# Kernel optimization log

Hardware: AMD Instinct MI355X
Metric: run time of the kernel (lower is better)

## Reference

```python
import jax, jax.numpy as jnp
import numpy as np

B, S = 2, 2048          # packed prefill: 2 sequences of 2048 tokens
T = B * S
HID = 3584
H, KV, D = 16, 8, 256   # query heads, kv heads, head_dim (num_groups = 2)
SCALE = 256.0 ** -0.5   # query_pre_attn_scalar ** -0.5
SOFTCAP = 50.0
WINDOW = 1024           # sliding_window (window_size_left)
ROPE_THETA = 10000.0


def _rope_cos_sin():
    # TGI PositionRotaryEmbedding: per-token cos/sin of shape [T, D//2]
    inv_freq = 1.0 / (ROPE_THETA ** (np.arange(0, D, 2, dtype=np.float32) / D))
    pos = np.tile(np.arange(S, dtype=np.float32), B)  # positions restart per sequence
    freqs = pos[:, None] * inv_freq[None, :]          # [T, D/2]
    return jnp.asarray(np.cos(freqs)), jnp.asarray(np.sin(freqs))


def _apply_rope(x, cos, sin):
    # neox-style rotate-half; x: [T, h, D], cos/sin: [T, D/2]
    x1, x2 = x[..., : D // 2], x[..., D // 2 :]
    c, s = cos[:, None, :], sin[:, None, :]
    return jnp.concatenate([x1 * c - x2 * s, x2 * c + x1 * s], axis=-1)


def setup_inputs() -> dict:
    key = jax.random.key(0)
    k1, k2, k3 = jax.random.split(key, 3)
    cos, sin = _rope_cos_sin()
    return {
        "hidden_states": jax.random.normal(k1, (T, HID), dtype=jnp.float32),
        "cos": cos,
        "sin": sin,
        "w_qkv": jax.random.normal(k2, ((H + 2 * KV) * D, HID), dtype=jnp.float32) * 0.02,
        "w_o": jax.random.normal(k3, (HID, H * D), dtype=jnp.float32) * 0.02,
    }


def reference(hidden_states, cos, sin, w_qkv, w_o):
    qkv = hidden_states @ w_qkv.T                      # [T, (H+2KV)*D]
    q = qkv[:, : H * D].reshape(T, H, D)
    k = qkv[:, H * D : (H + KV) * D].reshape(T, KV, D)
    v = qkv[:, (H + KV) * D :].reshape(T, KV, D)

    q = _apply_rope(q, cos, sin)
    k = _apply_rope(k, cos, sin)

    # unpack varlen batch (equal-length sequences)
    q = q.reshape(B, S, H, D)
    # GQA: repeat each kv head num_groups=2 times (kv_head_mapping)
    k = jnp.repeat(k.reshape(B, S, KV, D), H // KV, axis=2)
    v = jnp.repeat(v.reshape(B, S, KV, D), H // KV, axis=2)

    scores = jnp.einsum("bqhd,bkhd->bhqk", q, k) * SCALE
    scores = SOFTCAP * jnp.tanh(scores / SOFTCAP)      # logit softcapping

    i = jnp.arange(S)[:, None]
    j = jnp.arange(S)[None, :]
    allowed = (j <= i) & (j >= i - WINDOW)             # causal + sliding window left
    scores = jnp.where(allowed[None, None], scores, jnp.finfo(scores.dtype).min)

    probs = jax.nn.softmax(scores, axis=-1)
    out = jnp.einsum("bhqk,bkhd->bqhd", probs, v)      # [B, S, H, D]
    return out.reshape(T, H * D) @ w_o.T               # [T, HID]
```

## Files before the change

### kernel.cpp

```cpp
#include <hip/hip_runtime.h>

typedef __bf16 bf16x8 __attribute__((ext_vector_type(8)));
typedef __bf16 bf16x4 __attribute__((ext_vector_type(4)));
typedef float  f32x4  __attribute__((ext_vector_type(4)));

#define AS1 __attribute__((address_space(1)))
#define AS3 __attribute__((address_space(3)))

__device__ __forceinline__ void async16(const void* g, void* l) {
  __builtin_amdgcn_global_load_lds((const AS1 void*)g, (AS3 void*)l, 16, 0, 0);
}

static constexpr int T_   = 4096;
static constexpr int Sq   = 2048;
static constexpr int HID  = 3584;
static constexpr int NH   = 16;
static constexpr int NKV  = 8;
static constexpr int DH   = 256;
static constexpr float SCALE_   = 0.0625f;
static constexpr float SOFTCAP_ = 50.0f;
static constexpr int WINDOW_    = 1024;

__global__ __launch_bounds__(256) void cast2_f32_bf16(const float4* __restrict__ a,
                                                      bf16x4* __restrict__ oa, int n4a,
                                                      const float4* __restrict__ b,
                                                      bf16x4* __restrict__ ob, int n4b) {
  int i = blockIdx.x * 256 + threadIdx.x;
  int stride = gridDim.x * 256;
  int ntot = n4a + n4b;
  for (; i < ntot; i += stride) {
    const float4 v = (i < n4a) ? a[i] : b[i - n4a];
    bf16x4 o;
    o[0] = (__bf16)v.x; o[1] = (__bf16)v.y; o[2] = (__bf16)v.z; o[3] = (__bf16)v.w;
    if (i < n4a) oa[i] = o; else ob[i - n4a] = o;
  }
}

template <bool OUT_BF16>
__global__ __launch_bounds__(256) void gemm_bt(const __bf16* __restrict__ A,
                                               const __bf16* __restrict__ B,
                                               __bf16* __restrict__ Cb,
                                               float* __restrict__ Cf,
                                               int M, int N, int K) {
  __shared__ __bf16 lA[128 * 64];
  __shared__ __bf16 lB[128 * 64];
  const int tid  = threadIdx.x;
  const int w    = tid >> 6;
  const int lane = tid & 63;
  const int mrow = lane & 15;
  const int quad = lane >> 4;
  const int sw   = mrow & 7;
  const int tileN = blockIdx.x * 128;
  const int tileM = blockIdx.y * 128;
  const int wr = (w >> 1) * 64;
  const int wc = (w & 1) * 64;

  f32x4 acc[4][4];
#pragma unroll
  for (int i = 0; i < 4; ++i)
#pragma unroll
    for (int j = 0; j < 4; ++j) acc[i][j] = (f32x4){0.f, 0.f, 0.f, 0.f};

  const int rsub = tid >> 3;
  const int usw  = (tid & 7) ^ (rsub & 7);
  const int ccol = usw * 8;

  for (int k0 = 0; k0 < K; k0 += 64) {
#pragma unroll
    for (int it = 0; it < 4; ++it) {
      int row = it * 32 + rsub;
      const __bf16* ga = A + (size_t)(tileM + row) * K + k0 + ccol;
      const __bf16* gb = B + (size_t)(tileN + row) * K + k0 + ccol;
      async16(ga, &lA[(it * 256 + w * 64) * 8]);
      async16(gb, &lB[(it * 256 + w * 64) * 8]);
    }
    __syncthreads();
#pragma unroll
    for (int kk = 0; kk < 2; ++kk) {
      bf16x8 af[4], bfr[4];
#pragma unroll
      for (int i = 0; i < 4; ++i)
        af[i] = *(const bf16x8*)&lA[(wr + i * 16 + mrow) * 64 + (((kk * 4 + quad) ^ sw) * 8)];
#pragma unroll
      for (int j = 0; j < 4; ++j)
        bfr[j] = *(const bf16x8*)&lB[(wc + j * 16 + mrow) * 64 + (((kk * 4 + quad) ^ sw) * 8)];
#pragma unroll
      for (int i = 0; i < 4; ++i)
#pragma unroll
        for (int j = 0; j < 4; ++j)
          acc[i][j] = __builtin_amdgcn_mfma_f32_16x16x32_bf16(af[i], bfr[j], acc[i][j], 0, 0, 0);
    }
    __syncthreads();
  }

#pragma unroll
  for (int i = 0; i < 4; ++i) {
    int row0 = tileM + wr + i * 16 + quad * 4;
#pragma unroll
    for (int j = 0; j < 4; ++j) {
      int col = tileN + wc + j * 16 + mrow;
#pragma unroll
      for (int r = 0; r < 4; ++r) {
        if constexpr (OUT_BF16)
          Cb[(size_t)(row0 + r) * N + col] = (__bf16)acc[i][j][r];
        else
          Cf[(size_t)(row0 + r) * N + col] = acc[i][j][r];
      }
    }
  }
}

__global__ __launch_bounds__(256) void aux_fused(const __bf16* __restrict__ qkv,
                                                 const float* __restrict__ cosb,
                                                 const float* __restrict__ sinb,
                                                 __bf16* __restrict__ qout,
                                                 __bf16* __restrict__ kout,
                                                 __bf16* __restrict__ vt,
                                                 const float4* __restrict__ wo,
                                                 bf16x4* __restrict__ wo_bf) {
  __shared__ __bf16 tile[64][72];
  const int blk = blockIdx.x;
  const int tid = threadIdx.x;

  if (blk < 4096) {
    const int t = blk;
    const int b = t >> 11, s = t & (Sq - 1);
    const int d = tid & 127;
    const int half = tid >> 7;
    const float c  = cosb[t * 128 + d];
    const float sn = sinb[t * 128 + d];
    const size_t base = (size_t)t * 8192;
#pragma unroll
    for (int it = 0; it < 12; ++it) {
      int seg = it * 2 + half;
      float x1 = (float)qkv[base + seg * 256 + d];
      float x2 = (float)qkv[base + seg * 256 + 128 + d];
      float o1 = x1 * c - x2 * sn;
      float o2 = x2 * c + x1 * sn;
      if (seg < 16) {
        size_t o = ((size_t)(b * NH + seg) * Sq + s) * DH + d;
        qout[o] = (__bf16)o1;
        qout[o + 128] = (__bf16)o2;
      } else {
        int kvh = seg - 16;
        size_t o = ((size_t)(b * NKV + kvh) * Sq + s) * DH + d;
        kout[o] = (__bf16)o1;
        kout[o + 128] = (__bf16)o2;
      }
    }
  } else if (blk < 6144) {
    const int flat = blk - 4096;
    const int bx  = flat & 127;
    const int bkv = flat >> 7;
    const int b = bkv >> 3, kv = bkv & 7;
    const int st0 = (bx >> 2) * 64;
    const int dt0 = (bx & 3) * 64;
#pragma unroll
    for (int it = 0; it < 2; ++it) {
      int g = it * 256 + tid;
      int r = g >> 3, cc = (g & 7) * 8;
      const __bf16* src = qkv + (size_t)(b * Sq + st0 + r) * 8192 + 6144 + kv * 256 + dt0 + cc;
      bf16x8 v = *(const bf16x8*)src;
#pragma unroll
      for (int j = 0; j < 8; ++j) tile[r][cc + j] = v[j];
    }
    __syncthreads();
#pragma unroll
    for (int it = 0; it < 2; ++it) {
      int g = it * 256 + tid;
      int r = g >> 3, cc = (g & 7) * 8;
      bf16x8 v;
#pragma unroll
      for (int j = 0; j < 8; ++j) v[j] = tile[cc + j][r];
      *(bf16x8*)(vt + ((size_t)bkv * DH + dt0 + r) * Sq + st0 + cc) = v;
    }
  } else {
    const int n4 = HID * 4096 / 4;
    int i = (blk - 6144) * 256 + tid;
    const int stride = 1024 * 256;
    for (; i < n4; i += stride) {
      float4 v = wo[i];
      bf16x4 o;
      o[0] = (__bf16)v.x; o[1] = (__bf16)v.y; o[2] = (__bf16)v.z; o[3] = (__bf16)v.w;
      wo_bf[i] = o;
    }
  }
}

template <int MODE>
__device__ __forceinline__ void softcap_tile(const f32x4 sc[4], float lrun[4],
                                             __bf16* Pl, int pbase, int mrow,
                                             int kt, int qi) {
#pragma unroll
  for (int j = 0; j < 4; ++j) {
    const int kj = kt + j * 16 + mrow;
#pragma unroll
    for (int r = 0; r < 4; ++r) {
      float z = sc[j][r] * (SCALE_ / SOFTCAP_);
      float z2 = z * z;
      float u = __builtin_fmaf(z2, 0.13333333f, -0.33333333f);
      float th = z * __builtin_fmaf(z2, u, 1.0f);
      float pe = __builtin_fmaf(th, 72.134752f, -72.134752f);
      if (MODE == 1) pe = (kj <= qi + r) ? pe : -1000.0f;
      if (MODE == 2) pe = (kj >= qi + r - WINDOW_) ? pe : -1000.0f;
      float p = __builtin_amdgcn_exp2f(pe);
      lrun[r] += p;
      Pl[pbase + r * 72 + j * 16 + mrow] = (__bf16)p;
    }
  }
}

__global__ __launch_bounds__(256, 2) void attn_kernel(const __bf16* __restrict__ q,
                                                      const __bf16* __restrict__ k,
                                                      const __bf16* __restrict__ vt,
                                                      __bf16* __restrict__ out) {
  __shared__ __bf16 Kl[64 * 256];
  __shared__ __bf16 Vl[256 * 64];
  __shared__ __bf16 Pl[4 * 1152];

  const int bid0 = blockIdx.x;
  const int gidx = (bid0 & 7) * 128 + (bid0 >> 3);
  const int grp  = gidx >> 5;
  const int qt   = 31 - (gidx & 31);
  const int h    = grp & 15;
  const int b    = grp >> 4;
  const int kvh  = h >> 1;
  const int q0   = qt * 64;
  const int tid = threadIdx.x, w = tid >> 6, lane = tid & 63;
  const int mrow = lane & 15, quad = lane >> 4;
  const int sw = mrow & 7;

  bf16x8 qf[8];
  const __bf16* qbase = q + ((size_t)(b * NH + h) * Sq + q0 + w * 16 + mrow) * DH;
#pragma unroll
  for (int kf = 0; kf < 8; ++kf) qf[kf] = *(const bf16x8*)(qbase + kf * 32 + quad * 8);

  f32x4 o[16];
#pragma unroll
  for (int n = 0; n < 16; ++n) o[n] = (f32x4){0.f, 0.f, 0.f, 0.f};
  float lrun[4] = {0.f, 0.f, 0.f, 0.f};

  int kt_lo = q0 - WINDOW_; if (kt_lo < 0) kt_lo = 0;
  const __bf16* kbase = k + (size_t)(b * NKV + kvh) * Sq * DH;
  const __bf16* vbase = vt + (size_t)(b * NKV + kvh) * DH * Sq;
  const int qi = q0 + w * 16 + quad * 4;
  const int pbase = w * 1152 + quad * 4 * 72;

  for (int kt = kt_lo; kt <= q0; kt += 64) {
#pragma unroll
    for (int it = 0; it < 8; ++it) {
      int g = it * 256 + tid;
      int rk = g >> 5, uk = g & 31;
      const __bf16* gk = kbase + (size_t)(kt + rk) * DH + (uk ^ (rk & 7)) * 8;
      async16(gk, &Kl[(it * 256 + w * 64) * 8]);
    }
#pragma unroll
    for (int it = 0; it < 8; ++it) {
      int g = it * 256 + tid;
      int rv = g >> 3, uv = g & 7;
      const __bf16* gv = vbase + (size_t)rv * Sq + kt + (uv ^ (rv & 7)) * 8;
      async16(gv, &Vl[(it * 256 + w * 64) * 8]);
    }
    __syncthreads();

    f32x4 sc[4];
#pragma unroll
    for (int j = 0; j < 4; ++j) sc[j] = (f32x4){0.f, 0.f, 0.f, 0.f};
#pragma unroll
    for (int kf = 0; kf < 8; ++kf)
#pragma unroll
      for (int j = 0; j < 4; ++j) {
        bf16x8 kfr = *(const bf16x8*)&Kl[(j * 16 + mrow) * 256 + ((kf * 4 + quad) ^ sw) * 8];
        sc[j] = __builtin_amdgcn_mfma_f32_16x16x32_bf16(qf[kf], kfr, sc[j], 0, 0, 0);
      }

    if (kt == q0)                 softcap_tile<1>(sc, lrun, Pl, pbase, mrow, kt, qi);
    else if (kt == q0 - WINDOW_)  softcap_tile<2>(sc, lrun, Pl, pbase, mrow, kt, qi);
    else                          softcap_tile<0>(sc, lrun, Pl, pbase, mrow, kt, qi);

    bf16x8 pf0 = *(const bf16x8*)&Pl[w * 1152 + mrow * 72 + 0 * 32 + quad * 8];
    bf16x8 pf1 = *(const bf16x8*)&Pl[w * 1152 + mrow * 72 + 1 * 32 + quad * 8];

#pragma unroll
    for (int kk = 0; kk < 2; ++kk) {
      bf16x8 pf = kk ? pf1 : pf0;
#pragma unroll
      for (int n = 0; n < 16; ++n) {
        bf16x8 vf = *(const bf16x8*)&Vl[(n * 16 + mrow) * 64 + ((kk * 4 + quad) ^ sw) * 8];
        o[n] = __builtin_amdgcn_mfma_f32_16x16x32_bf16(pf, vf, o[n], 0, 0, 0);
      }
    }
    __syncthreads();
  }

#pragma unroll
  for (int m = 1; m < 16; m <<= 1)
#pragma unroll
    for (int r = 0; r < 4; ++r) lrun[r] += __shfl_xor(lrun[r], m, 64);

  float inv[4];
#pragma unroll
  for (int r = 0; r < 4; ++r) inv[r] = 1.f / lrun[r];
  const size_t trow = (size_t)(b * Sq + q0 + w * 16 + quad * 4);
#pragma unroll
  for (int n = 0; n < 16; ++n)
#pragma unroll
    for (int r = 0; r < 4; ++r)
      out[(trow + r) * 4096 + h * DH + n * 16 + mrow] = (__bf16)(o[n][r] * inv[r]);
}

extern "C" void kernel_launch(void* const* d_in, const int* in_sizes, int n_in,
                              void* d_out, int out_size, void* d_ws, size_t ws_size,
                              hipStream_t stream) {
  (void)in_sizes; (void)n_in; (void)out_size; (void)ws_size;
  const float* hs   = (const float*)d_in[0];
  const float* cosb = (const float*)d_in[1];
  const float* sinb = (const float*)d_in[2];
  const float* wqkv = (const float*)d_in[3];
  const float* wo   = (const float*)d_in[4];
  float* out = (float*)d_out;
  char* ws = (char*)d_ws;

  __bf16* hs_bf   = (__bf16*)(ws + 0);
  __bf16* wo_bf   = (__bf16*)(ws + 0);
  __bf16* wqkv_bf = (__bf16*)(ws + 29360128);
  __bf16* attn_bf = (__bf16*)(ws + 29360128);
  __bf16* qkv_bf  = (__bf16*)(ws + 88080384);
  __bf16* q_bf    = (__bf16*)(ws + 155189248);
  __bf16* k_bf    = (__bf16*)(ws + 188743680);
  __bf16* vt_bf   = (__bf16*)(ws + 205520896);

  cast2_f32_bf16<<<2048, 256, 0, stream>>>((const float4*)hs, (bf16x4*)hs_bf, T_ * HID / 4,
                                           (const float4*)wqkv, (bf16x4*)wqkv_bf, 8192 * HID / 4);

  gemm_bt<true><<<dim3(8192 / 128, T_ / 128), 256, 0, stream>>>(
      hs_bf, wqkv_bf, qkv_bf, nullptr, T_, 8192, HID);

  aux_fused<<<7168, 256, 0, stream>>>(qkv_bf, cosb, sinb, q_bf, k_bf, vt_bf,
                                      (const float4*)wo, (bf16x4*)wo_bf);

  attn_kernel<<<dim3(2 * NH * (Sq / 64)), 256, 0, stream>>>(q_bf, k_bf, vt_bf, attn_bf);

  gemm_bt<false><<<dim3(HID / 128, T_ / 128), 256, 0, stream>>>(
      attn_bf, wo_bf, nullptr, out, T_, HID, 4096);
}
```

Before: 802.5 us.

## Replace GEMM with 256x256 8-wave double-buffered pipelined kernel and XCD swizzle

Both projection GEMMs now use a new kernel with 256x256 tiles, 512 threads and double-buffered LDS. Global-to-LDS async loads for the next K tile are interleaved with MFMA phases, using explicit waitcnt, barriers and setprio. Workgroup IDs are remapped so neighbouring tiles land on the same XCD for better L2 reuse. The aim is to overlap memory with compute and raise arithmetic intensity. In exchange it uses 128KB of LDS, which limits occupancy, and tile-count imbalance may leave CUs idle at the grid tail (e.g. 14x16 tiles for the output GEMM).

New measurement: 743.2 us. 7.4% less time.

```diff
diff --git a/kernel.cpp b/kernel.cpp
--- a/kernel.cpp
+++ b/kernel.cpp
@@ -36,69 +36,159 @@
   }
 }
 
+
+#define PHASE_READS(BUFA, BUFB, I0, LOADB)                                         \
+  bf16x8 a_[2][2];                                                                 \
+  _Pragma("unroll") for (int ii_ = 0; ii_ < 2; ++ii_)                              \
+    _Pragma("unroll") for (int kk_ = 0; kk_ < 2; ++kk_)                            \
+      a_[ii_][kk_] = *(const bf16x8*)&BUFA[(wm * 128 + ((I0) + ii_) * 16 + mrow) * 64 \
+                                           + (((kk_ * 4 + quad) ^ sw) * 8)];       \
+  if (LOADB) {                                                                     \
+    _Pragma("unroll") for (int j_ = 0; j_ < 4; ++j_)                               \
+      _Pragma("unroll") for (int kk_ = 0; kk_ < 2; ++kk_)                          \
+        bfr[j_][kk_] = *(const bf16x8*)&BUFB[(wn * 64 + j_ * 16 + mrow) * 64       \
+                                             + (((kk_ * 4 + quad) ^ sw) * 8)];     \
+  }
+
+#define PHASE_MFMA(I0)                                                             \
+  __builtin_amdgcn_s_barrier();                                                    \
+  asm volatile("s_waitcnt lgkmcnt(0)" ::: "memory");                               \
+  __builtin_amdgcn_sched_barrier(0);                                               \
+  __builtin_amdgcn_s_setprio(1);                                                   \
+  _Pragma("unroll") for (int kk_ = 0; kk_ < 2; ++kk_)                              \
+    _Pragma("unroll") for (int ii_ = 0; ii_ < 2; ++ii_)                            \
+      _Pragma("unroll") for (int j_ = 0; j_ < 4; ++j_)                             \
+        acc[(I0) + ii_][j_] = __builtin_amdgcn_mfma_f32_16x16x32_bf16(             \
+            a_[ii_][kk_], bfr[j_][kk_], acc[(I0) + ii_][j_], 0, 0, 0);             \
+  __builtin_amdgcn_s_setprio(0);                                                   \
+  __builtin_amdgcn_sched_barrier(0);                                               \
+  __builtin_amdgcn_s_barrier();
+
 template <bool OUT_BF16>
-__global__ __launch_bounds__(256) void gemm_bt(const __bf16* __restrict__ A,
-                                               const __bf16* __restrict__ B,
-                                               __bf16* __restrict__ Cb,
-                                               float* __restrict__ Cf,
-                                               int M, int N, int K) {
-  __shared__ __bf16 lA[128 * 64];
-  __shared__ __bf16 lB[128 * 64];
+__global__ __launch_bounds__(512, 2) void gemm_bt8(const __bf16* __restrict__ A,
+                                                   const __bf16* __restrict__ B,
+                                                   __bf16* __restrict__ Cb,
+                                                   float* __restrict__ Cf,
+                                                   int M, int N, int K) {
+  __shared__ __attribute__((aligned(16))) __bf16 lA[2][256 * 64];
+  __shared__ __attribute__((aligned(16))) __bf16 lB[2][256 * 64];
+
   const int tid  = threadIdx.x;
   const int w    = tid >> 6;
   const int lane = tid & 63;
+  const int wm   = w >> 2;
+  const int wn   = w & 3;
   const int mrow = lane & 15;
   const int quad = lane >> 4;
   const int sw   = mrow & 7;
-  const int tileN = blockIdx.x * 128;
-  const int tileM = blockIdx.y * 128;
-  const int wr = (w >> 1) * 64;
-  const int wc = (w & 1) * 64;
-
-  f32x4 acc[4][4];
-#pragma unroll
-  for (int i = 0; i < 4; ++i)
+
+  const int nwg  = gridDim.x * gridDim.y;
+  const int orig = blockIdx.y * gridDim.x + blockIdx.x;
+  const int qq = nwg >> 3, rr = nwg & 7;
+  const int xcd = orig & 7, loc = orig >> 3;
+  const int swzb = (xcd < rr ? xcd * (qq + 1) : rr * (qq + 1) + (xcd - rr) * qq) + loc;
+  const int tileN = (swzb % gridDim.x) * 256;
+  const int tileM = (swzb / gridDim.x) * 256;
+
+  const int srow   = tid >> 3;
+  const int schunk = (tid & 7) ^ (srow & 7);
+
+  auto stage_half = [&](__bf16* lbase, int lrow, const __bf16* gptr, int grow, int kt) {
+#pragma unroll
+    for (int c = 0; c < 2; ++c) {
+      const __bf16* g = gptr + (size_t)(grow + c * 64 + srow) * K + kt + schunk * 8;
+      async16(g, &lbase[(lrow + c * 64 + w * 8) * 64]);
+    }
+  };
+
+  f32x4 acc[8][4];
+#pragma unroll
+  for (int i = 0; i < 8; ++i)
 #pragma unroll
     for (int j = 0; j < 4; ++j) acc[i][j] = (f32x4){0.f, 0.f, 0.f, 0.f};
 
-  const int rsub = tid >> 3;
-  const int usw  = (tid & 7) ^ (rsub & 7);
-  const int ccol = usw * 8;
-
-  for (int k0 = 0; k0 < K; k0 += 64) {
-#pragma unroll
-    for (int it = 0; it < 4; ++it) {
-      int row = it * 32 + rsub;
-      const __bf16* ga = A + (size_t)(tileM + row) * K + k0 + ccol;
-      const __bf16* gb = B + (size_t)(tileN + row) * K + k0 + ccol;
-      async16(ga, &lA[(it * 256 + w * 64) * 8]);
-      async16(gb, &lB[(it * 256 + w * 64) * 8]);
-    }
-    __syncthreads();
-#pragma unroll
-    for (int kk = 0; kk < 2; ++kk) {
-      bf16x8 af[4], bfr[4];
-#pragma unroll
-      for (int i = 0; i < 4; ++i)
-        af[i] = *(const bf16x8*)&lA[(wr + i * 16 + mrow) * 64 + (((kk * 4 + quad) ^ sw) * 8)];
-#pragma unroll
-      for (int j = 0; j < 4; ++j)
-        bfr[j] = *(const bf16x8*)&lB[(wc + j * 16 + mrow) * 64 + (((kk * 4 + quad) ^ sw) * 8)];
-#pragma unroll
-      for (int i = 0; i < 4; ++i)
-#pragma unroll
-        for (int j = 0; j < 4; ++j)
-          acc[i][j] = __builtin_amdgcn_mfma_f32_16x16x32_bf16(af[i], bfr[j], acc[i][j], 0, 0, 0);
-    }
-    __syncthreads();
-  }
-
-#pragma unroll
-  for (int i = 0; i < 4; ++i) {
-    int row0 = tileM + wr + i * 16 + quad * 4;
+  const int NT = K >> 6;
+  const int NI = NT >> 1;
+
+  stage_half(lB[0], 0,   B, tileN,       0);
+  stage_half(lB[0], 128, B, tileN + 128, 0);
+  stage_half(lA[0], 0,   A, tileM,       0);
+  stage_half(lA[0], 128, A, tileM + 128, 0);
+  stage_half(lB[1], 0,   B, tileN,       64);
+  stage_half(lB[1], 128, B, tileN + 128, 64);
+  asm volatile("s_waitcnt vmcnt(4)" ::: "memory");
+  __builtin_amdgcn_sched_barrier(0);
+  __builtin_amdgcn_s_barrier();
+
+  for (int it = 0; it < NI; ++it) {
+    const int t    = 2 * it;
+    const bool more = (it + 1 < NI);
+    const int kA1 = (t + 1) << 6;
+    const int k2  = (t + 2) << 6;
+    const int k3  = (t + 3) << 6;
+
+    bf16x8 bfr[4][2];
+
+    {
+      PHASE_READS(lA[0], lB[0], 0, true);
+      stage_half(lA[1], 0, A, tileM, kA1);
+      PHASE_MFMA(0);
+    }
+    {
+      PHASE_READS(lA[0], lB[0], 2, false);
+      stage_half(lA[1], 128, A, tileM + 128, kA1);
+      PHASE_MFMA(2);
+    }
+    {
+      PHASE_READS(lA[0], lB[0], 4, false);
+      if (more) stage_half(lB[0], 0, B, tileN, k2);
+      PHASE_MFMA(4);
+    }
+    {
+      PHASE_READS(lA[0], lB[0], 6, false);
+      if (more) {
+        stage_half(lB[0], 128, B, tileN + 128, k2);
+        asm volatile("s_waitcnt vmcnt(4)" ::: "memory");
+      } else {
+        asm volatile("s_waitcnt vmcnt(0)" ::: "memory");
+      }
+      __builtin_amdgcn_sched_barrier(0);
+      PHASE_MFMA(6);
+    }
+    {
+      PHASE_READS(lA[1], lB[1], 0, true);
+      if (more) stage_half(lA[0], 0, A, tileM, k2);
+      PHASE_MFMA(0);
+    }
+    {
+      PHASE_READS(lA[1], lB[1], 2, false);
+      if (more) stage_half(lA[0], 128, A, tileM + 128, k2);
+      PHASE_MFMA(2);
+    }
+    {
+      PHASE_READS(lA[1], lB[1], 4, false);
+      if (more) stage_half(lB[1], 0, B, tileN, k3);
+      PHASE_MFMA(4);
+    }
+    {
+      PHASE_READS(lA[1], lB[1], 6, false);
+      if (more) {
+        stage_half(lB[1], 128, B, tileN + 128, k3);
+        asm volatile("s_waitcnt vmcnt(4)" ::: "memory");
+      } else {
+        asm volatile("s_waitcnt vmcnt(0)" ::: "memory");
+      }
+      __builtin_amdgcn_sched_barrier(0);
+      PHASE_MFMA(6);
+    }
+  }
+
+#pragma unroll
+  for (int i = 0; i < 8; ++i) {
+    const int row0 = tileM + wm * 128 + i * 16 + quad * 4;
 #pragma unroll
     for (int j = 0; j < 4; ++j) {
-      int col = tileN + wc + j * 16 + mrow;
+      const int col = tileN + wn * 64 + j * 16 + mrow;
 #pragma unroll
       for (int r = 0; r < 4; ++r) {
         if constexpr (OUT_BF16)
@@ -333,7 +423,7 @@
   cast2_f32_bf16<<<2048, 256, 0, stream>>>((const float4*)hs, (bf16x4*)hs_bf, T_ * HID / 4,
                                            (const float4*)wqkv, (bf16x4*)wqkv_bf, 8192 * HID / 4);
 
-  gemm_bt<true><<<dim3(8192 / 128, T_ / 128), 256, 0, stream>>>(
+  gemm_bt8<true><<<dim3(8192 / 256, T_ / 256), 512, 0, stream>>>(
       hs_bf, wqkv_bf, qkv_bf, nullptr, T_, 8192, HID);
 
   aux_fused<<<7168, 256, 0, stream>>>(qkv_bf, cosb, sinb, q_bf, k_bf, vt_bf,
@@ -341,6 +431,6 @@
 
   attn_kernel<<<dim3(2 * NH * (Sq / 64)), 256, 0, stream>>>(q_bf, k_bf, vt_bf, attn_bf);
 
-  gemm_bt<false><<<dim3(HID / 128, T_ / 128), 256, 0, stream>>>(
+  gemm_bt8<false><<<dim3(HID / 256, T_ / 256), 512, 0, stream>>>(
       attn_bf, wo_bf, nullptr, out, T_, HID, 4096);
 }
```

## Replace GEMM with 256x256 double-buffered 8-wave pipelined kernel and XCD-aware tile mapping

Applied to the files above, without the earlier changes.

Replaces the 128x128 single-buffered GEMM with a 256x256 tile, 512-thread kernel that double-buffers LDS and interleaves async global-to-LDS loads with MFMA phases, using explicit waitcnt, barriers and setprio. Block indices are remapped so each XCD works on a contiguous region of the output, which should improve L2 reuse. The aim is to hide memory latency behind compute and raise arithmetic intensity in the QKV and output projections. The cost is 128KB of LDS per block and larger accumulator register use. Grid dimensions must also divide evenly: HID/256 = 14, and with gy = 16 the remap falls back to a 2x4 XCD split.

Result: faster. 701.9 us (-12.5%).

```diff
diff --git a/kernel.cpp b/kernel.cpp
--- a/kernel.cpp
+++ b/kernel.cpp
@@ -36,69 +36,142 @@
   }
 }
 
+
+#define VMW(N) do { asm volatile("s_waitcnt vmcnt(" #N ")" ::: "memory"); \
+                    __builtin_amdgcn_sched_barrier(0); } while (0)
+
+#define PHASE(SEL, CK, I0, KK, LOADB, STAGE)                                   \
+  {                                                                            \
+    bf16x8 a_[4];                                                              \
+    _Pragma("unroll") for (int ii_ = 0; ii_ < 4; ++ii_)                        \
+      a_[ii_] = *(const bf16x8*)&lA[SEL][aBase + (CK) + ((I0) + ii_) * 1024];  \
+    if (LOADB) {                                                               \
+      _Pragma("unroll") for (int j_ = 0; j_ < 4; ++j_)                         \
+        bfr[j_][KK] = *(const bf16x8*)&lB[SEL][bBase + (CK) + j_ * 1024];      \
+    }                                                                          \
+    STAGE;                                                                     \
+    __builtin_amdgcn_s_barrier();                                              \
+    asm volatile("s_waitcnt lgkmcnt(0)" ::: "memory");                         \
+    __builtin_amdgcn_sched_barrier(0);                                         \
+    __builtin_amdgcn_s_setprio(1);                                             \
+    _Pragma("unroll") for (int ii_ = 0; ii_ < 4; ++ii_)                        \
+      _Pragma("unroll") for (int j_ = 0; j_ < 4; ++j_)                         \
+        acc[(I0) + ii_][j_] = __builtin_amdgcn_mfma_f32_16x16x32_bf16(         \
+            a_[ii_], bfr[j_][KK], acc[(I0) + ii_][j_], 0, 0, 0);               \
+    __builtin_amdgcn_s_setprio(0);                                             \
+    __builtin_amdgcn_sched_barrier(0);                                         \
+    __builtin_amdgcn_s_barrier();                                              \
+  }
+
 template <bool OUT_BF16>
-__global__ __launch_bounds__(256) void gemm_bt(const __bf16* __restrict__ A,
-                                               const __bf16* __restrict__ B,
-                                               __bf16* __restrict__ Cb,
-                                               float* __restrict__ Cf,
-                                               int M, int N, int K) {
-  __shared__ __bf16 lA[128 * 64];
-  __shared__ __bf16 lB[128 * 64];
+__global__ __launch_bounds__(512, 2) void gemm_bt8(const __bf16* __restrict__ A,
+                                                   const __bf16* __restrict__ B,
+                                                   __bf16* __restrict__ Cb,
+                                                   float* __restrict__ Cf,
+                                                   int M, int N, int K) {
+  __shared__ __attribute__((aligned(16))) __bf16 lA[2][256 * 64];
+  __shared__ __attribute__((aligned(16))) __bf16 lB[2][256 * 64];
+
   const int tid  = threadIdx.x;
   const int w    = tid >> 6;
   const int lane = tid & 63;
+  const int wm   = w >> 2;
+  const int wn   = w & 3;
   const int mrow = lane & 15;
   const int quad = lane >> 4;
   const int sw   = mrow & 7;
-  const int tileN = blockIdx.x * 128;
-  const int tileM = blockIdx.y * 128;
-  const int wr = (w >> 1) * 64;
-  const int wc = (w & 1) * 64;
-
-  f32x4 acc[4][4];
-#pragma unroll
-  for (int i = 0; i < 4; ++i)
+
+  const int gx = gridDim.x, gy = gridDim.y;
+  const int orig = blockIdx.y * gx + blockIdx.x;
+  int tileN, tileM;
+  {
+    int ccols, crows;
+    if ((gx % 4) == 0 && (gy % 2) == 0)      { ccols = 4; crows = 2; }
+    else if ((gx % 2) == 0 && (gy % 4) == 0) { ccols = 2; crows = 4; }
+    else                                     { ccols = 1; crows = 1; }
+    if (ccols * crows == 8) {
+      const int cw = gx / ccols, ch = gy / crows;
+      const int xcd = orig & 7, loc = orig >> 3;
+      const int cx = xcd % ccols, cy = xcd / ccols;
+      const int ln = loc % cw,    lm = loc / cw;
+      tileN = (cx * cw + ln) * 256;
+      tileM = (cy * ch + lm) * 256;
+    } else {
+      tileN = blockIdx.x * 256;
+      tileM = blockIdx.y * 256;
+    }
+  }
+
+  const int srow   = tid >> 3;
+  const int schunk = (tid & 7) ^ (srow & 7);
+  const int k64  = K << 6;
+  const int k128 = K << 7;
+  const __bf16* pa = A + (size_t)(tileM + srow) * K + schunk * 8;
+  const __bf16* pb = B + (size_t)(tileN + srow) * K + schunk * 8;
+
+  auto stage_half = [&](__bf16* lbase, int lrow, const __bf16* lanePtr, int koff) {
+    async16(lanePtr + koff,       &lbase[(lrow + w * 8) * 64]);
+    async16(lanePtr + koff + k64, &lbase[(lrow + 64 + w * 8) * 64]);
+  };
+
+  const int cK0 = (quad ^ sw) * 8;
+  const int cK1 = cK0 ^ 32;
+  const int aBase = (wm * 128 + mrow) * 64;
+  const int bBase = (wn * 64 + mrow) * 64;
+
+  f32x4 acc[8][4];
+#pragma unroll
+  for (int i = 0; i < 8; ++i)
 #pragma unroll
     for (int j = 0; j < 4; ++j) acc[i][j] = (f32x4){0.f, 0.f, 0.f, 0.f};
 
-  const int rsub = tid >> 3;
-  const int usw  = (tid & 7) ^ (rsub & 7);
-  const int ccol = usw * 8;
-
-  for (int k0 = 0; k0 < K; k0 += 64) {
-#pragma unroll
-    for (int it = 0; it < 4; ++it) {
-      int row = it * 32 + rsub;
-      const __bf16* ga = A + (size_t)(tileM + row) * K + k0 + ccol;
-      const __bf16* gb = B + (size_t)(tileN + row) * K + k0 + ccol;
-      async16(ga, &lA[(it * 256 + w * 64) * 8]);
-      async16(gb, &lB[(it * 256 + w * 64) * 8]);
-    }
-    __syncthreads();
-#pragma unroll
-    for (int kk = 0; kk < 2; ++kk) {
-      bf16x8 af[4], bfr[4];
-#pragma unroll
-      for (int i = 0; i < 4; ++i)
-        af[i] = *(const bf16x8*)&lA[(wr + i * 16 + mrow) * 64 + (((kk * 4 + quad) ^ sw) * 8)];
-#pragma unroll
-      for (int j = 0; j < 4; ++j)
-        bfr[j] = *(const bf16x8*)&lB[(wc + j * 16 + mrow) * 64 + (((kk * 4 + quad) ^ sw) * 8)];
-#pragma unroll
-      for (int i = 0; i < 4; ++i)
-#pragma unroll
-        for (int j = 0; j < 4; ++j)
-          acc[i][j] = __builtin_amdgcn_mfma_f32_16x16x32_bf16(af[i], bfr[j], acc[i][j], 0, 0, 0);
-    }
-    __syncthreads();
-  }
-
-#pragma unroll
-  for (int i = 0; i < 4; ++i) {
-    int row0 = tileM + wr + i * 16 + quad * 4;
+  const int NT = K >> 6;
+  const int NI = NT >> 1;
+
+  stage_half(lB[0], 0,   pb, 0);
+  stage_half(lB[0], 128, pb, k128);
+  stage_half(lA[0], 0,   pa, 0);
+  stage_half(lA[0], 128, pa, k128);
+  stage_half(lB[1], 0,   pb, 64);
+  stage_half(lB[1], 128, pb, 64 + k128);
+  VMW(4);
+  __builtin_amdgcn_s_barrier();
+
+  for (int it = 0; it < NI; ++it) {
+    const int t    = 2 * it;
+    const bool more = (it + 1 < NI);
+    const int kA1 = (t + 1) << 6;
+    const int k2  = (t + 2) << 6;
+    const int k3  = (t + 3) << 6;
+
+    bf16x8 bfr[4][2];
+
+    PHASE(0, cK0, 0, 0, true,
+          { stage_half(lA[1], 0, pa, kA1); });
+    PHASE(0, cK1, 0, 1, true,
+          { stage_half(lA[1], 128, pa, kA1 + k128); });
+    PHASE(0, cK0, 4, 0, false,
+          { if (more) stage_half(lB[0], 0, pb, k2); });
+    PHASE(0, cK1, 4, 1, false,
+          { if (more) { stage_half(lB[0], 128, pb, k2 + k128); VMW(4); }
+            else VMW(0); });
+    PHASE(1, cK0, 0, 0, true,
+          { if (more) stage_half(lA[0], 0, pa, k2); });
+    PHASE(1, cK1, 0, 1, true,
+          { if (more) stage_half(lA[0], 128, pa, k2 + k128); });
+    PHASE(1, cK0, 4, 0, false,
+          { if (more) stage_half(lB[1], 0, pb, k3); });
+    PHASE(1, cK1, 4, 1, false,
+          { if (more) { stage_half(lB[1], 128, pb, k3 + k128); VMW(4); }
+            else VMW(0); });
+  }
+
+#pragma unroll
+  for (int i = 0; i < 8; ++i) {
+    const int row0 = tileM + wm * 128 + i * 16 + quad * 4;
 #pragma unroll
     for (int j = 0; j < 4; ++j) {
-      int col = tileN + wc + j * 16 + mrow;
+      const int col = tileN + wn * 64 + j * 16 + mrow;
 #pragma unroll
       for (int r = 0; r < 4; ++r) {
         if constexpr (OUT_BF16)
@@ -333,7 +406,7 @@
   cast2_f32_bf16<<<2048, 256, 0, stream>>>((const float4*)hs, (bf16x4*)hs_bf, T_ * HID / 4,
                                            (const float4*)wqkv, (bf16x4*)wqkv_bf, 8192 * HID / 4);
 
-  gemm_bt<true><<<dim3(8192 / 128, T_ / 128), 256, 0, stream>>>(
+  gemm_bt8<true><<<dim3(8192 / 256, T_ / 256), 512, 0, stream>>>(
       hs_bf, wqkv_bf, qkv_bf, nullptr, T_, 8192, HID);
 
   aux_fused<<<7168, 256, 0, stream>>>(qkv_bf, cosb, sinb, q_bf, k_bf, vt_bf,
@@ -341,6 +414,6 @@
 
   attn_kernel<<<dim3(2 * NH * (Sq / 64)), 256, 0, stream>>>(q_bf, k_bf, vt_bf, attn_bf);
 
-  gemm_bt<false><<<dim3(HID / 128, T_ / 128), 256, 0, stream>>>(
+  gemm_bt8<false><<<dim3(HID / 256, T_ / 256), 512, 0, stream>>>(
       attn_bf, wo_bf, nullptr, out, T_, HID, 4096);
 }
```
